# Optimization experiments

Hardware: AMD Instinct MI355X
Metric: run time of the kernel (lower is better)

The kernel has to match this reference:

```python
import jax, jax.numpy as jnp
import numpy as np

N = 512          # atoms
MAX_DIST = 16    # shortest-path truncation
N_HEADS = 32
N_SPATIAL = 64
BOND_TYPES = 32  # bond_types_number global in original repo


def setup_inputs() -> dict:
    key = jax.random.key(0)
    k1, k2, k3, k4, k5 = jax.random.split(key, 5)
    spatial_pos = jax.random.randint(k1, (N, N), 0, N_SPATIAL, dtype=jnp.int32)
    edge_input = jax.random.randint(k2, (N, N, MAX_DIST), 0, BOND_TYPES, dtype=jnp.int32)
    # embedding tables; padding_idx=0 -> zero row 0
    spd_table = jax.random.normal(k3, (N_SPATIAL, N_HEADS), dtype=jnp.float32).at[0].set(0.0)
    edge_table = jax.random.normal(k4, (BOND_TYPES, N_HEADS), dtype=jnp.float32).at[0].set(0.0)
    edge_dis_weight = jax.random.normal(k5, (N_SPATIAL * N_HEADS * N_HEADS, 1), dtype=jnp.float32)
    return {
        "spatial_pos": spatial_pos,
        "edge_input": edge_input,
        "max_dist": MAX_DIST,
        "spd_table": spd_table,
        "edge_table": edge_table,
        "edge_dis_weight": edge_dis_weight,
    }


def reference(spatial_pos, edge_input, max_dist, spd_table, edge_table, edge_dis_weight):
    n_heads = spd_table.shape[1]
    # phi_spd: embedding gather [n,n,H] -> [H,n,n]
    phi_spd = jnp.transpose(spd_table[spatial_pos], (2, 0, 1))
    # edge embedding gather: [n,n,D,H]
    edge_emb = edge_table[edge_input]
    # per-distance HxH weight matrices: [D,H,H]
    W = edge_dis_weight.reshape(-1, n_heads, n_heads)[:max_dist]
    # fused per-hop bmm + sum over hops: sum_d edge_emb[i,j,d,:] @ W[d]  -> [n,n,H]
    edge_sum = jnp.einsum('ijdh,dhk->ijk', edge_emb, W)
    # divide by clamped shortest-path distance (0 -> 1)
    denom = jnp.where(spatial_pos == 0, 1, spatial_pos).astype(edge_sum.dtype)[..., None]
    phi_edge = jnp.transpose(edge_sum / denom, (2, 0, 1))
    return (phi_spd, phi_edge)
```

## Files before the change

kernel.cpp:

```cpp
#include <hip/hip_runtime.h>
#include <hip/hip_fp16.h>
#include <stdint.h>

#define NH 32

__device__ __forceinline__ float bf_to_f(uint16_t u)
{
    return __uint_as_float(((uint32_t)u) << 16);
}

__device__ __forceinline__ void cp16(const void* g, void* l)
{
    __builtin_amdgcn_global_load_lds(
        (const __attribute__((address_space(1))) void*)g,
        (__attribute__((address_space(3))) void*)l, 16, 0, 0);
}

__device__ __forceinline__ int block_detect_fp32(const uint16_t* p16, int tid,
                                                 int* s_flag)
{
    if (tid == 0) *s_flag = 0;
    __syncthreads();
    const ushort4* p = (const ushort4*)p16;
    ushort4 a = p[tid * 2];
    ushort4 b = p[tid * 2 + 1];
    int big = 0;
    big |= (((a.x >> 7) & 0xFF) >= 0x89); big |= (((a.y >> 7) & 0xFF) >= 0x89);
    big |= (((a.z >> 7) & 0xFF) >= 0x89); big |= (((a.w >> 7) & 0xFF) >= 0x89);
    big |= (((b.x >> 7) & 0xFF) >= 0x89); big |= (((b.y >> 7) & 0xFF) >= 0x89);
    big |= (((b.z >> 7) & 0xFF) >= 0x89); big |= (((b.w >> 7) & 0xFF) >= 0x89);
    if (big) atomicOr(s_flag, 1);
    __syncthreads();
    return *s_flag;
}

__global__ __launch_bounds__(256) void prep(
    const void* __restrict__ edge_table,
    const void* __restrict__ W,
    const void* __restrict__ spd,
    uint16_t* __restrict__ T16,
    float* __restrict__ spdT,
    int totalT, int spd_n)
{
    __shared__ int s_flag;
    const int tid = threadIdx.x;
    const int is_fp32 = block_detect_fp32((const uint16_t*)spd, tid, &s_flag);
    int g = blockIdx.x * 256 + tid;
    if (g < totalT) {
        int d = g >> 10, e = (g >> 5) & 31, k = g & 31;
        float acc = 0.f;
        if (is_fp32) {
            const float* et = (const float*)edge_table + e * NH;
            const float* w  = (const float*)W + d * NH * NH + k;
#pragma unroll
            for (int h = 0; h < NH; ++h) acc += et[h] * w[h * NH];
        } else {
            const uint16_t* et = (const uint16_t*)edge_table + e * NH;
            const uint16_t* w  = (const uint16_t*)W + d * NH * NH + k;
#pragma unroll
            for (int h = 0; h < NH; ++h) acc += bf_to_f(et[h]) * bf_to_f(w[h * NH]);
        }
        int slot = (k >> 3) ^ ((e >> 1) & 3);
        int idx  = (((d << 5) | e) << 5) + (slot << 3) + (k & 7);
        __half hv = __float2half(acc);
        T16[idx] = *(const uint16_t*)&hv;
    } else {
        int i = g - totalT;
        if (i < spd_n) {
            float v = is_fp32 ? ((const float*)spd)[i]
                              : bf_to_f(((const uint16_t*)spd)[i]);
            int s = i >> 5, h = i & 31;
            spdT[h * (spd_n >> 5) + s] = v;
        }
    }
}

__global__ __launch_bounds__(256, 2) void bond2d(
    const int* __restrict__ spatial,
    const int* __restrict__ edge,
    const float4* __restrict__ SgT,
    const float4* __restrict__ Tg,
    float* __restrict__ out,
    int npairs, int D, int ns, int ntiles, int gridsz)
{
    __shared__ float4 Tl[2048];
    __shared__ float4 Sl4[512];
    const float* Sl = (const float*)Sl4;

    const int t = threadIdx.x;
    const bool small_ns = (ns <= 64);
    const float* SgTf = (const float*)SgT;

    for (int i = t; i < D * 128; i += 256)
        cp16(Tg + i, Tl + i);
    if (small_ns) {
        const int nsf4 = (NH * ns) >> 2;
        for (int i = t; i < nsf4; i += 256)
            cp16(SgT + i, Sl4 + i);
    }

    int tile = blockIdx.x;
    int  pc  = tile * 256 + t;
    bool vc  = (pc < npairs);
    int  pcc = vc ? pc : 0;
    int  sc  = spatial[pcc];
    int4 c0, c1, c2, c3;
    if (D == 16) {
        const int4* er = (const int4*)(edge + (size_t)pcc * 16);
        c0 = er[0]; c1 = er[1]; c2 = er[2]; c3 = er[3];
    }

    __syncthreads();

    if (D == 16) {
        for (;;) {
            const int  tn  = tile + gridsz;
            const bool hn  = (tn < ntiles);
            int  pn = tn * 256 + t;
            bool vn = hn && (pn < npairs);
            int  pnn = vn ? pn : 0;
            int  sn = 0;
            int4 n0, n1, n2, n3;
            if (hn) {
                sn = spatial[pnn];
                const int4* er = (const int4*)(edge + (size_t)pnn * 16);
                n0 = er[0]; n1 = er[1]; n2 = er[2]; n3 = er[3];
            }

            int ev[16];
            ev[0]=c0.x;  ev[1]=c0.y;  ev[2]=c0.z;  ev[3]=c0.w;
            ev[4]=c1.x;  ev[5]=c1.y;  ev[6]=c1.z;  ev[7]=c1.w;
            ev[8]=c2.x;  ev[9]=c2.y;  ev[10]=c2.z; ev[11]=c2.w;
            ev[12]=c3.x; ev[13]=c3.y; ev[14]=c3.z; ev[15]=c3.w;

            float acc[32];
#pragma unroll
            for (int k = 0; k < 32; ++k) acc[k] = 0.f;

            const char* Tb = (const char*)Tl;
#pragma unroll
            for (int d = 0; d < 16; ++d) {
                int e    = ev[d];
                int base = (((d << 5) | e) << 6);
                int s    = ((e >> 1) & 3) << 4;
#pragma unroll
                for (int m = 0; m < 4; ++m) {
                    uint4 w = *(const uint4*)(Tb + base + ((m << 4) ^ s));
                    float2 f0 = __half22float2(*(const __half2*)&w.x);
                    float2 f1 = __half22float2(*(const __half2*)&w.y);
                    float2 f2 = __half22float2(*(const __half2*)&w.z);
                    float2 f3 = __half22float2(*(const __half2*)&w.w);
                    acc[8*m+0] += f0.x; acc[8*m+1] += f0.y;
                    acc[8*m+2] += f1.x; acc[8*m+3] += f1.y;
                    acc[8*m+4] += f2.x; acc[8*m+5] += f2.y;
                    acc[8*m+6] += f3.x; acc[8*m+7] += f3.y;
                }
            }

            if (vc) {
                const float rs = 1.0f / (sc ? (float)sc : 1.0f);
                float* o0 = out + pc;
                float* o1 = out + (size_t)NH * npairs + pc;
                const float* sA = Sl + sc;
#pragma unroll
                for (int k = 0; k < 32; ++k) {
                    o1[(size_t)k * npairs] = acc[k] * rs;
                    o0[(size_t)k * npairs] =
                        small_ns ? sA[k * ns] : SgTf[(size_t)k * ns + sc];
                }
            }

            if (!hn) break;
            tile = tn; pc = pn; vc = vn; pcc = pnn; sc = sn;
            c0 = n0; c1 = n1; c2 = n2; c3 = n3;
        }
    } else {
        for (; tile < ntiles; tile += gridsz) {
            int  p  = tile * 256 + t;
            bool v  = (p < npairs);
            int  pp = v ? p : 0;
            int  s  = spatial[pp];
            const int* erow = edge + (size_t)pp * D;

            float acc[32];
#pragma unroll
            for (int k = 0; k < 32; ++k) acc[k] = 0.f;

            const char* Tb = (const char*)Tl;
            for (int d = 0; d < D; ++d) {
                int e    = erow[d];
                int base = (((d << 5) | e) << 6);
                int sw   = ((e >> 1) & 3) << 4;
#pragma unroll
                for (int m = 0; m < 4; ++m) {
                    uint4 w = *(const uint4*)(Tb + base + ((m << 4) ^ sw));
                    float2 f0 = __half22float2(*(const __half2*)&w.x);
                    float2 f1 = __half22float2(*(const __half2*)&w.y);
                    float2 f2 = __half22float2(*(const __half2*)&w.z);
                    float2 f3 = __half22float2(*(const __half2*)&w.w);
                    acc[8*m+0] += f0.x; acc[8*m+1] += f0.y;
                    acc[8*m+2] += f1.x; acc[8*m+3] += f1.y;
                    acc[8*m+4] += f2.x; acc[8*m+5] += f2.y;
                    acc[8*m+6] += f3.x; acc[8*m+7] += f3.y;
                }
            }

            if (v) {
                const float rs = 1.0f / (s ? (float)s : 1.0f);
                float* o0 = out + p;
                float* o1 = out + (size_t)NH * npairs + p;
                const float* sA = Sl + s;
#pragma unroll
                for (int k = 0; k < 32; ++k) {
                    o1[(size_t)k * npairs] = acc[k] * rs;
                    o0[(size_t)k * npairs] =
                        small_ns ? sA[k * ns] : SgTf[(size_t)k * ns + s];
                }
            }
        }
    }
}

extern "C" void kernel_launch(void* const* d_in, const int* in_sizes, int n_in,
                              void* d_out, int out_size, void* d_ws, size_t ws_size,
                              hipStream_t stream) {
    const int* spatial = (const int*)d_in[0];
    const int* edge    = (const int*)d_in[1];
    const void* spd    = d_in[3];
    const void* etab   = d_in[4];
    const void* W      = d_in[5];

    long long npairs = in_sizes[0];
    long long etot   = in_sizes[1];
    int D = (int)(etot / (npairs > 0 ? npairs : 1));
    if (D < 1) D = 1;
    if (D > 16) D = 16;
    int spd_n  = in_sizes[3];
    int ns     = spd_n >> 5;
    int totalT = D * 1024;

    uint16_t* T16 = (uint16_t*)d_ws;
    float*    spdT = (float*)(T16 + totalT);

    prep<<<(totalT + spd_n + 255) / 256, 256, 0, stream>>>(
        etab, W, spd, T16, spdT, totalT, spd_n);

    int ntiles = (int)((npairs + 255) / 256);
    int gridsz = ntiles < 512 ? ntiles : 512;
    bond2d<<<gridsz, 256, 0, stream>>>(spatial, edge, (const float4*)spdT,
                                       (const float4*)T16, (float*)d_out,
                                       (int)npairs, D, ns, ntiles, gridsz);
}
```

Before: 102.1 us.

## Split heads across two thread halves so each tile covers 128 pairs

Each block now assigns two threads per atom pair, with each thread accumulating 16 of the 32 heads instead of all 32. This halves accumulator registers per thread and doubles the number of tiles, which is meant to raise occupancy and parallelism for the LDS-gather-bound inner loop. In exchange, both threads of a pair load the same spatial and edge indices redundantly, doubling global index traffic, and the XOR swizzle now applies to a 32-byte offset.

```diff
diff --git a/kernel.cpp b/kernel.cpp
--- a/kernel.cpp
+++ b/kernel.cpp
@@ -87,7 +87,9 @@
     __shared__ float4 Sl4[512];
     const float* Sl = (const float*)Sl4;
 
-    const int t = threadIdx.x;
+    const int t  = threadIdx.x;
+    const int kh = t >> 7;
+    const int lp = t & 127;
     const bool small_ns = (ns <= 64);
     const float* SgTf = (const float*)SgT;
 
@@ -100,7 +102,7 @@
     }
 
     int tile = blockIdx.x;
-    int  pc  = tile * 256 + t;
+    int  pc  = tile * 128 + lp;
     bool vc  = (pc < npairs);
     int  pcc = vc ? pc : 0;
     int  sc  = spatial[pcc];
@@ -116,7 +118,7 @@
         for (;;) {
             const int  tn  = tile + gridsz;
             const bool hn  = (tn < ntiles);
-            int  pn = tn * 256 + t;
+            int  pn = tn * 128 + lp;
             bool vn = hn && (pn < npairs);
             int  pnn = vn ? pn : 0;
             int  sn = 0;
@@ -133,40 +135,42 @@
             ev[8]=c2.x;  ev[9]=c2.y;  ev[10]=c2.z; ev[11]=c2.w;
             ev[12]=c3.x; ev[13]=c3.y; ev[14]=c3.z; ev[15]=c3.w;
 
-            float acc[32];
-#pragma unroll
-            for (int k = 0; k < 32; ++k) acc[k] = 0.f;
+            float acc[16];
+#pragma unroll
+            for (int k = 0; k < 16; ++k) acc[k] = 0.f;
 
             const char* Tb = (const char*)Tl;
+            const int mbase = kh << 5;
 #pragma unroll
             for (int d = 0; d < 16; ++d) {
                 int e    = ev[d];
                 int base = (((d << 5) | e) << 6);
-                int s    = ((e >> 1) & 3) << 4;
-#pragma unroll
-                for (int m = 0; m < 4; ++m) {
-                    uint4 w = *(const uint4*)(Tb + base + ((m << 4) ^ s));
+                int sw   = ((e >> 1) & 3) << 4;
+#pragma unroll
+                for (int mm = 0; mm < 2; ++mm) {
+                    uint4 w = *(const uint4*)(Tb + base + ((mbase + (mm << 4)) ^ sw));
                     float2 f0 = __half22float2(*(const __half2*)&w.x);
                     float2 f1 = __half22float2(*(const __half2*)&w.y);
                     float2 f2 = __half22float2(*(const __half2*)&w.z);
                     float2 f3 = __half22float2(*(const __half2*)&w.w);
-                    acc[8*m+0] += f0.x; acc[8*m+1] += f0.y;
-                    acc[8*m+2] += f1.x; acc[8*m+3] += f1.y;
-                    acc[8*m+4] += f2.x; acc[8*m+5] += f2.y;
-                    acc[8*m+6] += f3.x; acc[8*m+7] += f3.y;
+                    acc[8*mm+0] += f0.x; acc[8*mm+1] += f0.y;
+                    acc[8*mm+2] += f1.x; acc[8*mm+3] += f1.y;
+                    acc[8*mm+4] += f2.x; acc[8*mm+5] += f2.y;
+                    acc[8*mm+6] += f3.x; acc[8*mm+7] += f3.y;
                 }
             }
 
             if (vc) {
                 const float rs = 1.0f / (sc ? (float)sc : 1.0f);
+                const int hb = kh * 16;
                 float* o0 = out + pc;
                 float* o1 = out + (size_t)NH * npairs + pc;
-                const float* sA = Sl + sc;
-#pragma unroll
-                for (int k = 0; k < 32; ++k) {
-                    o1[(size_t)k * npairs] = acc[k] * rs;
-                    o0[(size_t)k * npairs] =
-                        small_ns ? sA[k * ns] : SgTf[(size_t)k * ns + sc];
+#pragma unroll
+                for (int j = 0; j < 16; ++j) {
+                    o1[(size_t)(hb + j) * npairs] = acc[j] * rs;
+                    o0[(size_t)(hb + j) * npairs] =
+                        small_ns ? Sl[(hb + j) * ns + sc]
+                                 : SgTf[(size_t)(hb + j) * ns + sc];
                 }
             }
 
@@ -176,45 +180,47 @@
         }
     } else {
         for (; tile < ntiles; tile += gridsz) {
-            int  p  = tile * 256 + t;
+            int  p  = tile * 128 + lp;
             bool v  = (p < npairs);
             int  pp = v ? p : 0;
             int  s  = spatial[pp];
             const int* erow = edge + (size_t)pp * D;
 
-            float acc[32];
-#pragma unroll
-            for (int k = 0; k < 32; ++k) acc[k] = 0.f;
+            float acc[16];
+#pragma unroll
+            for (int k = 0; k < 16; ++k) acc[k] = 0.f;
 
             const char* Tb = (const char*)Tl;
+            const int mbase = kh << 5;
             for (int d = 0; d < D; ++d) {
                 int e    = erow[d];
                 int base = (((d << 5) | e) << 6);
                 int sw   = ((e >> 1) & 3) << 4;
 #pragma unroll
-                for (int m = 0; m < 4; ++m) {
-                    uint4 w = *(const uint4*)(Tb + base + ((m << 4) ^ sw));
+                for (int mm = 0; mm < 2; ++mm) {
+                    uint4 w = *(const uint4*)(Tb + base + ((mbase + (mm << 4)) ^ sw));
                     float2 f0 = __half22float2(*(const __half2*)&w.x);
                     float2 f1 = __half22float2(*(const __half2*)&w.y);
                     float2 f2 = __half22float2(*(const __half2*)&w.z);
                     float2 f3 = __half22float2(*(const __half2*)&w.w);
-                    acc[8*m+0] += f0.x; acc[8*m+1] += f0.y;
-                    acc[8*m+2] += f1.x; acc[8*m+3] += f1.y;
-                    acc[8*m+4] += f2.x; acc[8*m+5] += f2.y;
-                    acc[8*m+6] += f3.x; acc[8*m+7] += f3.y;
+                    acc[8*mm+0] += f0.x; acc[8*mm+1] += f0.y;
+                    acc[8*mm+2] += f1.x; acc[8*mm+3] += f1.y;
+                    acc[8*mm+4] += f2.x; acc[8*mm+5] += f2.y;
+                    acc[8*mm+6] += f3.x; acc[8*mm+7] += f3.y;
                 }
             }
 
             if (v) {
                 const float rs = 1.0f / (s ? (float)s : 1.0f);
+                const int hb = kh * 16;
                 float* o0 = out + p;
                 float* o1 = out + (size_t)NH * npairs + p;
-                const float* sA = Sl + s;
-#pragma unroll
-                for (int k = 0; k < 32; ++k) {
-                    o1[(size_t)k * npairs] = acc[k] * rs;
-                    o0[(size_t)k * npairs] =
-                        small_ns ? sA[k * ns] : SgTf[(size_t)k * ns + s];
+#pragma unroll
+                for (int j = 0; j < 16; ++j) {
+                    o1[(size_t)(hb + j) * npairs] = acc[j] * rs;
+                    o0[(size_t)(hb + j) * npairs] =
+                        small_ns ? Sl[(hb + j) * ns + s]
+                                 : SgTf[(size_t)(hb + j) * ns + s];
                 }
             }
         }
@@ -245,7 +251,7 @@
     prep<<<(totalT + spd_n + 255) / 256, 256, 0, stream>>>(
         etab, W, spd, T16, spdT, totalT, spd_n);
 
-    int ntiles = (int)((npairs + 255) / 256);
+    int ntiles = (int)((npairs + 127) / 128);
     int gridsz = ntiles < 512 ? ntiles : 512;
     bond2d<<<gridsz, 256, 0, stream>>>(spatial, edge, (const float4*)spdT,
                                        (const float4*)T16, (float*)d_out,
```

Result: slower. 105.2 us (+3.1%).
